# Kernel tuning notes

Measured on AMD Instinct MI355X. Metric: run time of the kernel, lower is better.

The kernel has to match this reference:

```python
import jax, jax.numpy as jnp
import numpy as np


def setup_inputs() -> dict:
    key = jax.random.key(0)
    ks = jax.random.split(key, 6)
    B = 65536
    x = jax.random.normal(ks[0], (B, 784), dtype=jnp.float32)
    conv_w = jax.random.normal(ks[1], (3, 3), dtype=jnp.float32)
    fc1_w = jax.random.normal(ks[2], (100, 676), dtype=jnp.float32) * (1.0 / np.sqrt(676))
    fc1_b = jax.random.normal(ks[3], (100,), dtype=jnp.float32) * 0.01
    fc2_w = jax.random.normal(ks[4], (10, 100), dtype=jnp.float32) * (1.0 / np.sqrt(100))
    fc2_b = jax.random.normal(ks[5], (10,), dtype=jnp.float32) * 0.01
    return {"x": x, "conv_w": conv_w, "fc1_w": fc1_w, "fc1_b": fc1_b, "fc2_w": fc2_w, "fc2_b": fc2_b}


def reference(x, conv_w, fc1_w, fc1_b, fc2_w, fc2_b):
    B = x.shape[0]
    img = x.reshape(B, 1, 28, 28)  # NCHW, single channel
    kern = conv_w.reshape(1, 1, 3, 3)  # OIHW
    # 'valid' cross-correlation, matching the slicing-based Convolve()
    conv = jax.lax.conv_general_dilated(
        img, kern, window_strides=(1, 1), padding='VALID',
        dimension_numbers=('NCHW', 'OIHW', 'NCHW'))  # [B,1,26,26]
    h = conv.reshape(B, 26 * 26)
    h = jax.nn.relu(h @ fc1_w.T + fc1_b)
    out = h @ fc2_w.T + fc2_b
    return out
```

## Files before the change

kernel.cpp:

```cpp
#include <hip/hip_runtime.h>


typedef short  s16x8  __attribute__((ext_vector_type(8)));
typedef float  f32x16 __attribute__((ext_vector_type(16)));

#define BM   32
#define CSTR 712
#define HSTR 132
#define NT   4
#define KC   43

__device__ __forceinline__ unsigned short f2bf(float f) {
    unsigned int u = __builtin_bit_cast(unsigned int, f);
    u = (u + 0x7fffu + ((u >> 16) & 1u)) >> 16;
    return (unsigned short)u;
}

extern "C" __global__ void __launch_bounds__(256)
prep_w1(const float* __restrict__ W1, const float* __restrict__ b1,
        unsigned short* __restrict__ bw)
{
    int id = blockIdx.x * 256 + threadIdx.x;
    if (id >= NT * KC * 64) return;
    int lane = id & 63;
    int kc   = (id >> 6) % KC;
    int t    = id / (KC * 64);
    int n    = t * 32 + (lane & 31);
    int k0   = kc * 16 + (lane >> 5) * 8;
    unsigned short v[8];
#pragma unroll
    for (int j = 0; j < 8; ++j) {
        int k = k0 + j;
        float f = 0.f;
        if (n < 100) {
            if (k < 676)       f = W1[(size_t)n * 676 + k];
            else if (k == 676) f = b1[n];
        }
        v[j] = f2bf(f);
    }
    *(uint4*)(bw + (size_t)id * 8) = *(const uint4*)v;
}

extern "C" __global__ void __launch_bounds__(512, 6)
digit_model_fused(const float* __restrict__ x,
                  const float* __restrict__ cw9,
                  const unsigned short* __restrict__ bw,
                  const float* __restrict__ W2,
                  const float* __restrict__ b2,
                  float* __restrict__ out)
{
    __shared__ __align__(16) unsigned char smem[BM * CSTR * 2];
    unsigned short* cbuf = (unsigned short*)smem;
    float* pbuf = (float*)smem;
    float* hbuf = (float*)(smem + 16384);

    const int tid  = threadIdx.x;
    const int lane = tid & 63;
    const int wv   = tid >> 6;
    const int t    = wv & 3;
    const int half = lane >> 5;
    const int ln   = lane & 31;
    const int m0   = blockIdx.x * BM;

    float cw[9];
#pragma unroll
    for (int i = 0; i < 9; ++i) cw[i] = cw9[i];

    for (int p = tid; p < BM * 18; p += 512) {
        int mi = p / 18, q = p - mi * 18;
        *(unsigned int*)(cbuf + mi * CSTR + 676 + q * 2) = (q == 0) ? 0x3F80u : 0u;
    }

    for (int task = tid; task < BM * 26; task += 512) {
        int mi = task / 26, r = task - mi * 26;
        const float* ip = x + (size_t)(m0 + mi) * 784 + r * 28;
        float acc[26];
#pragma unroll
        for (int c = 0; c < 26; ++c) acc[c] = 0.f;
#pragma unroll
        for (int dr = 0; dr < 3; ++dr) {
            float rowv[28];
            const float4* rp = (const float4*)(ip + dr * 28);
#pragma unroll
            for (int q = 0; q < 7; ++q) {
                float4 v = rp[q];
                rowv[q*4+0] = v.x; rowv[q*4+1] = v.y;
                rowv[q*4+2] = v.z; rowv[q*4+3] = v.w;
            }
#pragma unroll
            for (int dc = 0; dc < 3; ++dc) {
                float w = cw[dr*3+dc];
#pragma unroll
                for (int c = 0; c < 26; ++c) acc[c] = fmaf(rowv[c+dc], w, acc[c]);
            }
        }
        unsigned short* dst = cbuf + mi * CSTR + r * 26;
#pragma unroll
        for (int c = 0; c < 26; c += 2) {
            unsigned int u = (unsigned int)f2bf(acc[c])
                           | ((unsigned int)f2bf(acc[c+1]) << 16);
            *(unsigned int*)(dst + c) = u;
        }
    }
    __syncthreads();

    const int kbeg = (wv < 4) ? 0 : 21;
    const int kend = (wv < 4) ? 21 : KC;

    f32x16 acc;
#pragma unroll
    for (int i = 0; i < 16; ++i) acc[i] = 0.f;

    const unsigned short* arow = cbuf + ln * CSTR + half * 8;
    const uint4* bwv = (const uint4*)bw;

    uint4 araw = *(const uint4*)(arow + kbeg * 16);
    uint4 braw = bwv[(t * KC + kbeg) * 64 + lane];
    for (int kc = kbeg; kc < kend; ++kc) {
        int kn = (kc + 1 < kend) ? kc + 1 : kc;
        uint4 na = *(const uint4*)(arow + kn * 16);
        uint4 nb = bwv[(t * KC + kn) * 64 + lane];
        acc = __builtin_amdgcn_mfma_f32_32x32x16_bf16(
                  __builtin_bit_cast(s16x8, araw),
                  __builtin_bit_cast(s16x8, braw), acc, 0, 0, 0);
        araw = na; braw = nb;
    }
    __syncthreads();

    if (wv >= 4) {
#pragma unroll
        for (int r = 0; r < 16; ++r) {
            int row = (r & 3) + 8 * (r >> 2) + 4 * half;
            pbuf[t * 1024 + row * 32 + ln] = acc[r];
        }
    }
    __syncthreads();
    if (wv < 4) {
#pragma unroll
        for (int r = 0; r < 16; ++r) {
            int row = (r & 3) + 8 * (r >> 2) + 4 * half;
            float v = acc[r] + pbuf[t * 1024 + row * 32 + ln];
            v = v > 0.f ? v : 0.f;
            hbuf[row * HSTR + t * 32 + ln] = v;
        }
    }
    __syncthreads();

    for (int p = tid; p < BM * 10; p += 512) {
        int mi = p / 10, o = p - mi * 10;
        const float4* hv = (const float4*)(hbuf + mi * HSTR);
        const float4* w2 = (const float4*)(W2 + (size_t)o * 100);
        float s = b2[o];
#pragma unroll
        for (int q = 0; q < 25; ++q) {
            float4 h4 = hv[q], w4 = w2[q];
            s += h4.x*w4.x + h4.y*w4.y + h4.z*w4.z + h4.w*w4.w;
        }
        out[(size_t)(m0 + mi) * 10 + o] = s;
    }
}

extern "C" void kernel_launch(void* const* d_in, const int* in_sizes, int n_in,
                              void* d_out, int out_size, void* d_ws, size_t ws_size,
                              hipStream_t stream) {
    const float* x  = (const float*)d_in[0];
    const float* cw = (const float*)d_in[1];
    const float* W1 = (const float*)d_in[2];
    const float* b1 = (const float*)d_in[3];
    const float* W2 = (const float*)d_in[4];
    const float* b2 = (const float*)d_in[5];
    float* out = (float*)d_out;
    unsigned short* bw = (unsigned short*)d_ws;

    const int B = in_sizes[0] / 784;

    hipLaunchKernelGGL(prep_w1, dim3((NT * KC * 64 + 255) / 256), dim3(256),
                       0, stream, W1, b1, bw);
    hipLaunchKernelGGL(digit_model_fused, dim3(B / BM), dim3(512), 0, stream,
                       x, cw, bw, W2, b2, out);
}
```

Measured before the change: 348.2 us.

## Switch to 16-row tiles with 16x16x32 MFMA and no split-K reduction

Halves the batch tile to 16 rows and uses 256-thread blocks. The FC1 GEMM now uses 16x16x32 bf16 MFMA, with each wave owning two N-tiles over the full K range, which removes the split-K partial-sum pass through LDS and one barrier. The weight prepack layout changes to match. The convolution is split into half-row tasks so all threads stay busy with the smaller tile. The cost is twice as many blocks and less reuse of the weights per block.

```diff
diff --git a/kernel.cpp b/kernel.cpp
--- a/kernel.cpp
+++ b/kernel.cpp
@@ -1,14 +1,14 @@
 #include <hip/hip_runtime.h>
 
 
-typedef short  s16x8  __attribute__((ext_vector_type(8)));
-typedef float  f32x16 __attribute__((ext_vector_type(16)));
+typedef short  s16x8 __attribute__((ext_vector_type(8)));
+typedef float  f32x4 __attribute__((ext_vector_type(4)));
 
-#define BM   32
+#define BM   16
 #define CSTR 712
 #define HSTR 132
-#define NT   4
-#define KC   43
+#define NT   8
+#define KC   22
 
 __device__ __forceinline__ unsigned short f2bf(float f) {
     unsigned int u = __builtin_bit_cast(unsigned int, f);
@@ -25,8 +25,8 @@
     int lane = id & 63;
     int kc   = (id >> 6) % KC;
     int t    = id / (KC * 64);
-    int n    = t * 32 + (lane & 31);
-    int k0   = kc * 16 + (lane >> 5) * 8;
+    int n    = t * 16 + (lane & 15);
+    int k0   = kc * 32 + (lane >> 4) * 8;
     unsigned short v[8];
 #pragma unroll
     for (int j = 0; j < 8; ++j) {
@@ -41,7 +41,7 @@
     *(uint4*)(bw + (size_t)id * 8) = *(const uint4*)v;
 }
 
-extern "C" __global__ void __launch_bounds__(512, 6)
+extern "C" __global__ void __launch_bounds__(256, 6)
 digit_model_fused(const float* __restrict__ x,
                   const float* __restrict__ cw9,
                   const unsigned short* __restrict__ bw,
@@ -51,109 +51,109 @@
 {
     __shared__ __align__(16) unsigned char smem[BM * CSTR * 2];
     unsigned short* cbuf = (unsigned short*)smem;
-    float* pbuf = (float*)smem;
-    float* hbuf = (float*)(smem + 16384);
+    float*          hbuf = (float*)smem;
 
     const int tid  = threadIdx.x;
     const int lane = tid & 63;
     const int wv   = tid >> 6;
-    const int t    = wv & 3;
-    const int half = lane >> 5;
-    const int ln   = lane & 31;
+    const int q    = lane >> 4;
+    const int mn   = lane & 15;
     const int m0   = blockIdx.x * BM;
 
     float cw[9];
 #pragma unroll
     for (int i = 0; i < 9; ++i) cw[i] = cw9[i];
 
-    for (int p = tid; p < BM * 18; p += 512) {
-        int mi = p / 18, q = p - mi * 18;
-        *(unsigned int*)(cbuf + mi * CSTR + 676 + q * 2) = (q == 0) ? 0x3F80u : 0u;
+    for (int p = tid; p < BM * 18; p += 256) {
+        int mi = p / 18, qq = p - mi * 18;
+        *(unsigned int*)(cbuf + mi * CSTR + 676 + qq * 2) = (qq == 0) ? 0x3F80u : 0u;
     }
 
-    for (int task = tid; task < BM * 26; task += 512) {
-        int mi = task / 26, r = task - mi * 26;
-        const float* ip = x + (size_t)(m0 + mi) * 784 + r * 28;
-        float acc[26];
+    for (int task = tid; task < BM * 52; task += 256) {
+        int mi = task / 52, rh = task - mi * 52, r = rh >> 1, h = rh & 1;
+        const float* ip = x + (size_t)(m0 + mi) * 784 + r * 28 + h * 12;
+        float acc[13];
 #pragma unroll
-        for (int c = 0; c < 26; ++c) acc[c] = 0.f;
+        for (int c = 0; c < 13; ++c) acc[c] = 0.f;
 #pragma unroll
         for (int dr = 0; dr < 3; ++dr) {
-            float rowv[28];
+            float rowv[16];
             const float4* rp = (const float4*)(ip + dr * 28);
 #pragma unroll
-            for (int q = 0; q < 7; ++q) {
-                float4 v = rp[q];
-                rowv[q*4+0] = v.x; rowv[q*4+1] = v.y;
-                rowv[q*4+2] = v.z; rowv[q*4+3] = v.w;
+            for (int g = 0; g < 4; ++g) {
+                float4 v = rp[g];
+                rowv[g*4+0] = v.x; rowv[g*4+1] = v.y;
+                rowv[g*4+2] = v.z; rowv[g*4+3] = v.w;
             }
 #pragma unroll
             for (int dc = 0; dc < 3; ++dc) {
                 float w = cw[dr*3+dc];
 #pragma unroll
-                for (int c = 0; c < 26; ++c) acc[c] = fmaf(rowv[c+dc], w, acc[c]);
+                for (int c = 0; c < 13; ++c)
+                    acc[c] = fmaf(rowv[c + dc + h], w, acc[c]);
             }
         }
-        unsigned short* dst = cbuf + mi * CSTR + r * 26;
+        unsigned short* dst = cbuf + mi * CSTR + r * 26 + h * 13;
+        if (h == 0) {
 #pragma unroll
-        for (int c = 0; c < 26; c += 2) {
-            unsigned int u = (unsigned int)f2bf(acc[c])
-                           | ((unsigned int)f2bf(acc[c+1]) << 16);
-            *(unsigned int*)(dst + c) = u;
+            for (int c = 0; c < 12; c += 2)
+                *(unsigned int*)(dst + c) =
+                    (unsigned int)f2bf(acc[c]) | ((unsigned int)f2bf(acc[c+1]) << 16);
+            dst[12] = f2bf(acc[12]);
+        } else {
+            dst[0] = f2bf(acc[0]);
+#pragma unroll
+            for (int c = 1; c < 13; c += 2)
+                *(unsigned int*)(dst + c) =
+                    (unsigned int)f2bf(acc[c]) | ((unsigned int)f2bf(acc[c+1]) << 16);
         }
     }
     __syncthreads();
 
-    const int kbeg = (wv < 4) ? 0 : 21;
-    const int kend = (wv < 4) ? 21 : KC;
+    f32x4 acc0, acc1;
+#pragma unroll
+    for (int i = 0; i < 4; ++i) { acc0[i] = 0.f; acc1[i] = 0.f; }
 
-    f32x16 acc;
-#pragma unroll
-    for (int i = 0; i < 16; ++i) acc[i] = 0.f;
+    const unsigned short* arow = cbuf + mn * CSTR + q * 8;
+    const uint4* bwv = (const uint4*)bw;
+    const int t0 = wv, t1 = wv + 4;
 
-    const unsigned short* arow = cbuf + ln * CSTR + half * 8;
-    const uint4* bwv = (const uint4*)bw;
-
-    uint4 araw = *(const uint4*)(arow + kbeg * 16);
-    uint4 braw = bwv[(t * KC + kbeg) * 64 + lane];
-    for (int kc = kbeg; kc < kend; ++kc) {
-        int kn = (kc + 1 < kend) ? kc + 1 : kc;
-        uint4 na = *(const uint4*)(arow + kn * 16);
-        uint4 nb = bwv[(t * KC + kn) * 64 + lane];
-        acc = __builtin_amdgcn_mfma_f32_32x32x16_bf16(
-                  __builtin_bit_cast(s16x8, araw),
-                  __builtin_bit_cast(s16x8, braw), acc, 0, 0, 0);
-        araw = na; braw = nb;
+    uint4 a  = *(const uint4*)(arow);
+    uint4 b0 = bwv[(t0 * KC) * 64 + lane];
+    uint4 b1 = bwv[(t1 * KC) * 64 + lane];
+    for (int kc = 0; kc < KC; ++kc) {
+        int kn = (kc + 1 < KC) ? kc + 1 : kc;
+        uint4 na  = *(const uint4*)(arow + kn * 32);
+        uint4 nb0 = bwv[(t0 * KC + kn) * 64 + lane];
+        uint4 nb1 = bwv[(t1 * KC + kn) * 64 + lane];
+        acc0 = __builtin_amdgcn_mfma_f32_16x16x32_bf16(
+                   __builtin_bit_cast(s16x8, a), __builtin_bit_cast(s16x8, b0),
+                   acc0, 0, 0, 0);
+        acc1 = __builtin_amdgcn_mfma_f32_16x16x32_bf16(
+                   __builtin_bit_cast(s16x8, a), __builtin_bit_cast(s16x8, b1),
+                   acc1, 0, 0, 0);
+        a = na; b0 = nb0; b1 = nb1;
     }
     __syncthreads();
 
-    if (wv >= 4) {
 #pragma unroll
-        for (int r = 0; r < 16; ++r) {
-            int row = (r & 3) + 8 * (r >> 2) + 4 * half;
-            pbuf[t * 1024 + row * 32 + ln] = acc[r];
-        }
-    }
-    __syncthreads();
-    if (wv < 4) {
-#pragma unroll
-        for (int r = 0; r < 16; ++r) {
-            int row = (r & 3) + 8 * (r >> 2) + 4 * half;
-            float v = acc[r] + pbuf[t * 1024 + row * 32 + ln];
-            v = v > 0.f ? v : 0.f;
-            hbuf[row * HSTR + t * 32 + ln] = v;
-        }
+    for (int r = 0; r < 4; ++r) {
+        int row = q * 4 + r;
+        float v0 = acc0[r]; v0 = v0 > 0.f ? v0 : 0.f;
+        float v1 = acc1[r]; v1 = v1 > 0.f ? v1 : 0.f;
+        hbuf[row * HSTR + t0 * 16 + mn] = v0;
+        hbuf[row * HSTR + t1 * 16 + mn] = v1;
     }
     __syncthreads();
 
-    for (int p = tid; p < BM * 10; p += 512) {
+    for (int p = tid; p < BM * 10; p += 256) {
         int mi = p / 10, o = p - mi * 10;
         const float4* hv = (const float4*)(hbuf + mi * HSTR);
         const float4* w2 = (const float4*)(W2 + (size_t)o * 100);
         float s = b2[o];
 #pragma unroll
-        for (int q = 0; q < 25; ++q) {
-            float4 h4 = hv[q], w4 = w2[q];
+        for (int g = 0; g < 25; ++g) {
+            float4 h4 = hv[g], w4 = w2[g];
             s += h4.x*w4.x + h4.y*w4.y + h4.z*w4.z + h4.w*w4.w;
         }
         out[(size_t)(m0 + mi) * 10 + o] = s;
@@ -176,6 +176,6 @@
 
     hipLaunchKernelGGL(prep_w1, dim3((NT * KC * 64 + 255) / 256), dim3(256),
                        0, stream, W1, b1, bw);
-    hipLaunchKernelGGL(digit_model_fused, dim3(B / BM), dim3(512), 0, stream,
+    hipLaunchKernelGGL(digit_model_fused, dim3(B / BM), dim3(256), 0, stream,
                        x, cw, bw, W2, b2, out);
 }
```

Measured after the change: 327.8 us. 1.06x faster.
